# Kernel optimization log

Measured on AMD Instinct MI355X. Metric: run time of the kernel, lower is better.

Reference implementation:

```python
import jax, jax.numpy as jnp
import numpy as np

BATCH = 2048
DIMS = [256, 256, 256, 128]  # input, hidden, hidden, output
N_ATOMS = 4  # identity, sin, tanh, square


def setup_inputs() -> dict:
    key = jax.random.key(0)
    ks = jax.random.split(key, 8)
    inp = {"x": jax.random.normal(ks[0], (BATCH, DIMS[0]), dtype=jnp.float32)}
    for li in range(3):
        out_d, in_d = DIMS[li + 1], DIMS[li]
        inp[f"W{li}"] = jax.random.normal(ks[1 + li], (out_d, in_d), dtype=jnp.float32) * 0.1
        inp[f"b{li}"] = jnp.zeros((out_d,), dtype=jnp.float32)
        inp[f"f_idx{li}"] = jax.random.randint(ks[4 + li], (out_d, in_d), 0, N_ATOMS, dtype=jnp.int32)
    return inp


def _w_eff(W, idx):
    # per-element atom nonlinearity selected by idx: [identity, sin, tanh, square]
    atoms = jnp.stack([W, jnp.sin(W), jnp.tanh(W), W * W], axis=0)  # [A, out, in]
    return jnp.take_along_axis(atoms, idx[None].astype(jnp.int32), axis=0)[0]


def reference(x, W0, b0, W1, b1, W2, b2, f_idx0, f_idx1, f_idx2):
    layers = [(W0, b0, f_idx0), (W1, b1, f_idx1), (W2, b2, f_idx2)]
    h = x
    n = len(layers)
    for li, (W, b, idx) in enumerate(layers):
        We = _w_eff(W, idx)                       # [out, in]
        z = h[:, None, :] * We[None, :, :]        # [batch, out, in]
        gz = z if li == n - 1 else jnp.tanh(z)    # g_fixed='tanh' on hidden layers
        h = gz.sum(axis=-1) + b[None, :]          # [batch, out]
    return h
```

## Files before the change

### kernel.cpp

```cpp
#include <hip/hip_runtime.h>
#include <math.h>


typedef float v2f __attribute__((ext_vector_type(2)));

#define HCLAMP 12.0f
#define INV2PI 0.15915494309189535f
#define SCW    2.885390081777927f

__device__ __forceinline__ float fast_rcp(float x)  { return __builtin_amdgcn_rcpf(x); }
__device__ __forceinline__ float fast_exp2(float x) { return __builtin_amdgcn_exp2f(x); }
__device__ __forceinline__ v2f pk2(float a, float b) { v2f r; r.x = a; r.y = b; return r; }
__device__ __forceinline__ v2f splat2(float f) { v2f r; r.x = f; r.y = f; return r; }
__device__ __forceinline__ v2f vfma(v2f a, v2f b, v2f c) {
    return __builtin_elementwise_fma(a, b, c);
}

__global__ void weff_kernel(const float* __restrict__ W0, const int* __restrict__ I0,
                            const float* __restrict__ W1, const int* __restrict__ I1,
                            const float* __restrict__ W2, const int* __restrict__ I2,
                            float* __restrict__ ws) {
    int tid = blockIdx.x * blockDim.x + threadIdx.x;
    const float* W; const int* I; float* out; int outd; int e;
    if (tid < 65536)        { W = W0; I = I0; out = ws;          outd = 256; e = tid; }
    else if (tid < 131072)  { W = W1; I = I1; out = ws + 65536;  outd = 256; e = tid - 65536; }
    else if (tid < 163840)  { W = W2; I = I2; out = ws + 131072; outd = 128; e = tid - 131072; }
    else return;
    int o = e >> 8;
    int i = e & 255;
    float w = W[e];
    int idx = I[e];
    float sn = __builtin_amdgcn_sinf(w * INV2PI);
    float th = 1.0f - 2.0f * fast_rcp(fast_exp2(w * SCW) + 1.0f);
    float sq = w * w;
    float v = (idx == 1) ? sn : (idx == 2) ? th : (idx == 3) ? sq : w;
    out[(i >> 2) * (outd * 4) + o * 4 + (i & 3)] = v;
}

struct ND { v2f n, d; };
__device__ __forceinline__ ND pade1(v2f z) {
    const v2f c105 = splat2(105.0f), c945 = splat2(945.0f);
    const v2f c420 = splat2(420.0f), c15  = splat2(15.0f);
    v2f t = z * z;
    ND r;
    r.n = z * vfma(t, t + c105, c945);
    r.d = vfma(t, vfma(t, c15, c420), c945);
    return r;
}
__device__ __forceinline__ ND nd_merge(ND a, ND b) {
    ND r;
    r.n = vfma(a.n, b.d, b.n * a.d);
    r.d = a.d * b.d;
    return r;
}
__device__ __forceinline__ ND tree4(float4 pa, float4 pb, float4 w) {
    v2f h0 = pk2(pa.x, pa.y), h1 = pk2(pa.z, pa.w);
    v2f h2 = pk2(pb.x, pb.y), h3 = pk2(pb.z, pb.w);
    ND r0 = pade1(h0 * splat2(w.x));
    ND r1 = pade1(h1 * splat2(w.y));
    ND r2 = pade1(h2 * splat2(w.z));
    ND r3 = pade1(h3 * splat2(w.w));
    return nd_merge(nd_merge(r0, r1), nd_merge(r2, r3));
}
__device__ __forceinline__ v2f sig8_acc(ND a, ND b, v2f acc) {
    v2f num = vfma(b.n, a.d, a.n * b.d);
    v2f den = a.d * b.d;
    v2f rd;  rd.x = fast_rcp(den.x); rd.y = fast_rcp(den.y);
    return vfma(num, rd, acc);
}

__global__ __launch_bounds__(1024, 4) void mlp_kernel(
    const float* __restrict__ x,  const float* __restrict__ b0,
    const float* __restrict__ b1, const float* __restrict__ b2,
    const float* __restrict__ ws, float* __restrict__ out) {
    const float4* We0 = (const float4*)ws;
    const float4* We1 = (const float4*)(ws + 65536);
    const float4* We2 = (const float4*)(ws + 131072);

    __shared__ __align__(16) v2f hA0[256];
    __shared__ __align__(16) v2f hA1[256];
    __shared__ __align__(16) v2f hB0[256];
    __shared__ __align__(16) v2f hB1[256];
    __shared__ __align__(16) v2f partA[1024];
    __shared__ __align__(16) v2f partB[1024];

    const int t = threadIdx.x;
    const int g = t >> 8;
    const int o = t & 255;
    const int p = g >> 1;
    const int l = g & 1;
    const int row0 = blockIdx.x * 4;

    {
        float xv = x[(row0 + 2 * p + l) * 256 + o];
        xv = fminf(fmaxf(xv, -HCLAMP), HCLAMP);
        ((float*)((p ? hA1 : hA0) + o))[l] = xv;
    }
    __syncthreads();

    {
        const float bias = b0[o];
        v2f acc0 = splat2(0.f), acc1 = splat2(0.f);
#pragma unroll 1
        for (int icc = 0; icc < 16; icc += 2) {
            int ic = g * 16 + icc;
            float4 w0 = We0[ic * 256 + o];
            float4 w1 = We0[(ic + 1) * 256 + o];
            const float4* hp0 = (const float4*)(hA0 + ic * 4);
            const float4* hp1 = (const float4*)(hA1 + ic * 4);
            ND r0 = tree4(hp0[0], hp0[1], w0);
            ND r1 = tree4(hp0[2], hp0[3], w1);
            acc0 = sig8_acc(r0, r1, acc0);
            ND r2 = tree4(hp1[0], hp1[1], w0);
            ND r3 = tree4(hp1[2], hp1[3], w1);
            acc1 = sig8_acc(r2, r3, acc1);
        }
        partA[g * 256 + o] = acc0;
        partB[g * 256 + o] = acc1;
        __syncthreads();
        const v2f* prt = p ? partB : partA;
        float s = ((const float*)(prt + o))[l]
                + ((const float*)(prt + 256 + o))[l]
                + ((const float*)(prt + 512 + o))[l]
                + ((const float*)(prt + 768 + o))[l];
        float h = s + bias;
        h = fminf(fmaxf(h, -HCLAMP), HCLAMP);
        ((float*)((p ? hB1 : hB0) + o))[l] = h;
        __syncthreads();
    }

    {
        const float bias = b1[o];
        v2f acc0 = splat2(0.f), acc1 = splat2(0.f);
#pragma unroll 1
        for (int icc = 0; icc < 16; icc += 2) {
            int ic = g * 16 + icc;
            float4 w0 = We1[ic * 256 + o];
            float4 w1 = We1[(ic + 1) * 256 + o];
            const float4* hp0 = (const float4*)(hB0 + ic * 4);
            const float4* hp1 = (const float4*)(hB1 + ic * 4);
            ND r0 = tree4(hp0[0], hp0[1], w0);
            ND r1 = tree4(hp0[2], hp0[3], w1);
            acc0 = sig8_acc(r0, r1, acc0);
            ND r2 = tree4(hp1[0], hp1[1], w0);
            ND r3 = tree4(hp1[2], hp1[3], w1);
            acc1 = sig8_acc(r2, r3, acc1);
        }
        partA[g * 256 + o] = acc0;
        partB[g * 256 + o] = acc1;
        __syncthreads();
        const v2f* prt = p ? partB : partA;
        float s = ((const float*)(prt + o))[l]
                + ((const float*)(prt + 256 + o))[l]
                + ((const float*)(prt + 512 + o))[l]
                + ((const float*)(prt + 768 + o))[l];
        float h = s + bias;
        h = fminf(fmaxf(h, -HCLAMP), HCLAMP);
        ((float*)((p ? hB1 : hA0) + o))[l] = h;
        __syncthreads();
    }

    {
        const int o2 = t & 127;
        const int q  = t >> 7;
        v2f acc0 = splat2(0.f), acc1 = splat2(0.f);
#pragma unroll 4
        for (int icc = 0; icc < 8; icc++) {
            int ic = q * 8 + icc;
            float4 w = We2[ic * 128 + o2];
            const float4* hp0 = (const float4*)(hA0 + ic * 4);
            const float4* hp1 = (const float4*)(hB1 + ic * 4);
            float4 pa = hp0[0], pb = hp0[1];
            float4 qa = hp1[0], qb = hp1[1];
            acc0 = vfma(pk2(pa.x, pa.y), splat2(w.x), acc0);
            acc0 = vfma(pk2(pa.z, pa.w), splat2(w.y), acc0);
            acc0 = vfma(pk2(pb.x, pb.y), splat2(w.z), acc0);
            acc0 = vfma(pk2(pb.z, pb.w), splat2(w.w), acc0);
            acc1 = vfma(pk2(qa.x, qa.y), splat2(w.x), acc1);
            acc1 = vfma(pk2(qa.z, qa.w), splat2(w.y), acc1);
            acc1 = vfma(pk2(qb.x, qb.y), splat2(w.z), acc1);
            acc1 = vfma(pk2(qb.z, qb.w), splat2(w.w), acc1);
        }
        partA[q * 128 + o2] = acc0;
        partB[q * 128 + o2] = acc1;
        __syncthreads();
        if (t < 512) {
            const int r  = t >> 7;
            const int oo = t & 127;
            const v2f* prt = (r & 2) ? partB : partA;
            const int  ln  = r & 1;
            float s = 0.0f;
#pragma unroll
            for (int q2 = 0; q2 < 8; q2++)
                s += ((const float*)(prt + q2 * 128 + oo))[ln];
            out[(row0 + r) * 128 + oo] = s + b2[oo];
        }
    }
}

extern "C" void kernel_launch(void* const* d_in, const int* in_sizes, int n_in,
                              void* d_out, int out_size, void* d_ws, size_t ws_size,
                              hipStream_t stream) {
    const float* x  = (const float*)d_in[0];
    const float* W0 = (const float*)d_in[1];
    const float* b0 = (const float*)d_in[2];
    const int*   I0 = (const int*)  d_in[3];
    const float* W1 = (const float*)d_in[4];
    const float* b1 = (const float*)d_in[5];
    const int*   I1 = (const int*)  d_in[6];
    const float* W2 = (const float*)d_in[7];
    const float* b2 = (const float*)d_in[8];
    const int*   I2 = (const int*)  d_in[9];
    float* ws  = (float*)d_ws;
    float* out = (float*)d_out;

    weff_kernel<<<640, 256, 0, stream>>>(W0, I0, W1, I1, W2, I2, ws);
    mlp_kernel<<<512, 1024, 0, stream>>>(x, b0, b1, b2, ws, out);
}
```

Measured before the change: 126.4 us.

## Assign one row per thread group and drop the cross-group K-split reduction

Work is redistributed so each group of 256 threads owns one batch row and loops over the full input dimension. This removes the shared-memory partial-sum buffers and the extra barrier reductions per layer, and packs the v2f pairs along K instead of across two rows. In exchange each weight float4 is reused by one row instead of two, which doubles the weight loads per FLOP. The final layer also idles half the threads. The launch bound is relaxed from 4 to 2.

```diff
diff --git a/kernel.cpp b/kernel.cpp
--- a/kernel.cpp
+++ b/kernel.cpp
@@ -7,6 +7,7 @@
 #define HCLAMP 12.0f
 #define INV2PI 0.15915494309189535f
 #define SCW    2.885390081777927f
+#define LPAD   260
 
 __device__ __forceinline__ float fast_rcp(float x)  { return __builtin_amdgcn_rcpf(x); }
 __device__ __forceinline__ float fast_exp2(float x) { return __builtin_amdgcn_exp2f(x); }
@@ -53,15 +54,6 @@
     r.d = a.d * b.d;
     return r;
 }
-__device__ __forceinline__ ND tree4(float4 pa, float4 pb, float4 w) {
-    v2f h0 = pk2(pa.x, pa.y), h1 = pk2(pa.z, pa.w);
-    v2f h2 = pk2(pb.x, pb.y), h3 = pk2(pb.z, pb.w);
-    ND r0 = pade1(h0 * splat2(w.x));
-    ND r1 = pade1(h1 * splat2(w.y));
-    ND r2 = pade1(h2 * splat2(w.z));
-    ND r3 = pade1(h3 * splat2(w.w));
-    return nd_merge(nd_merge(r0, r1), nd_merge(r2, r3));
-}
 __device__ __forceinline__ v2f sig8_acc(ND a, ND b, v2f acc) {
     v2f num = vfma(b.n, a.d, a.n * b.d);
     v2f den = a.d * b.d;
@@ -69,7 +61,7 @@
     return vfma(num, rd, acc);
 }
 
-__global__ __launch_bounds__(1024, 4) void mlp_kernel(
+__global__ __launch_bounds__(1024, 2) void mlp_kernel(
     const float* __restrict__ x,  const float* __restrict__ b0,
     const float* __restrict__ b1, const float* __restrict__ b2,
     const float* __restrict__ ws, float* __restrict__ out) {
@@ -77,124 +69,75 @@
     const float4* We1 = (const float4*)(ws + 65536);
     const float4* We2 = (const float4*)(ws + 131072);
 
-    __shared__ __align__(16) v2f hA0[256];
-    __shared__ __align__(16) v2f hA1[256];
-    __shared__ __align__(16) v2f hB0[256];
-    __shared__ __align__(16) v2f hB1[256];
-    __shared__ __align__(16) v2f partA[1024];
-    __shared__ __align__(16) v2f partB[1024];
+    __shared__ __align__(16) float hA[4 * LPAD];
+    __shared__ __align__(16) float hB[4 * LPAD];
 
     const int t = threadIdx.x;
-    const int g = t >> 8;
+    const int r = t >> 8;
     const int o = t & 255;
-    const int p = g >> 1;
-    const int l = g & 1;
     const int row0 = blockIdx.x * 4;
 
     {
-        float xv = x[(row0 + 2 * p + l) * 256 + o];
-        xv = fminf(fmaxf(xv, -HCLAMP), HCLAMP);
-        ((float*)((p ? hA1 : hA0) + o))[l] = xv;
+        float xv = x[(row0 + r) * 256 + o];
+        hA[r * LPAD + o] = fminf(fmaxf(xv, -HCLAMP), HCLAMP);
     }
     __syncthreads();
 
     {
         const float bias = b0[o];
-        v2f acc0 = splat2(0.f), acc1 = splat2(0.f);
-#pragma unroll 1
-        for (int icc = 0; icc < 16; icc += 2) {
-            int ic = g * 16 + icc;
-            float4 w0 = We0[ic * 256 + o];
-            float4 w1 = We0[(ic + 1) * 256 + o];
-            const float4* hp0 = (const float4*)(hA0 + ic * 4);
-            const float4* hp1 = (const float4*)(hA1 + ic * 4);
-            ND r0 = tree4(hp0[0], hp0[1], w0);
-            ND r1 = tree4(hp0[2], hp0[3], w1);
-            acc0 = sig8_acc(r0, r1, acc0);
-            ND r2 = tree4(hp1[0], hp1[1], w0);
-            ND r3 = tree4(hp1[2], hp1[3], w1);
-            acc1 = sig8_acc(r2, r3, acc1);
+        const float* hr = hA + r * LPAD;
+        v2f acc = splat2(0.f);
+#pragma unroll 2
+        for (int kk = 0; kk < 64; kk += 2) {
+            float4 w0v = We0[kk * 256 + o];
+            float4 w1v = We0[(kk + 1) * 256 + o];
+            float4 h0v = *(const float4*)(hr + kk * 4);
+            float4 h1v = *(const float4*)(hr + kk * 4 + 4);
+            ND a = nd_merge(pade1(pk2(h0v.x, h0v.y) * pk2(w0v.x, w0v.y)),
+                            pade1(pk2(h0v.z, h0v.w) * pk2(w0v.z, w0v.w)));
+            ND b = nd_merge(pade1(pk2(h1v.x, h1v.y) * pk2(w1v.x, w1v.y)),
+                            pade1(pk2(h1v.z, h1v.w) * pk2(w1v.z, w1v.w)));
+            acc = sig8_acc(a, b, acc);
         }
-        partA[g * 256 + o] = acc0;
-        partB[g * 256 + o] = acc1;
-        __syncthreads();
-        const v2f* prt = p ? partB : partA;
-        float s = ((const float*)(prt + o))[l]
-                + ((const float*)(prt + 256 + o))[l]
-                + ((const float*)(prt + 512 + o))[l]
-                + ((const float*)(prt + 768 + o))[l];
-        float h = s + bias;
+        float h = acc.x + acc.y + bias;
         h = fminf(fmaxf(h, -HCLAMP), HCLAMP);
-        ((float*)((p ? hB1 : hB0) + o))[l] = h;
-        __syncthreads();
+        hB[r * LPAD + o] = h;
     }
+    __syncthreads();
 
     {
         const float bias = b1[o];
-        v2f acc0 = splat2(0.f), acc1 = splat2(0.f);
-#pragma unroll 1
-        for (int icc = 0; icc < 16; icc += 2) {
-            int ic = g * 16 + icc;
-            float4 w0 = We1[ic * 256 + o];
-            float4 w1 = We1[(ic + 1) * 256 + o];
-            const float4* hp0 = (const float4*)(hB0 + ic * 4);
-            const float4* hp1 = (const float4*)(hB1 + ic * 4);
-            ND r0 = tree4(hp0[0], hp0[1], w0);
-            ND r1 = tree4(hp0[2], hp0[3], w1);
-            acc0 = sig8_acc(r0, r1, acc0);
-            ND r2 = tree4(hp1[0], hp1[1], w0);
-            ND r3 = tree4(hp1[2], hp1[3], w1);
-            acc1 = sig8_acc(r2, r3, acc1);
+        const float* hr = hB + r * LPAD;
+        v2f acc = splat2(0.f);
+#pragma unroll 2
+        for (int kk = 0; kk < 64; kk += 2) {
+            float4 w0v = We1[kk * 256 + o];
+            float4 w1v = We1[(kk + 1) * 256 + o];
+            float4 h0v = *(const float4*)(hr + kk * 4);
+            float4 h1v = *(const float4*)(hr + kk * 4 + 4);
+            ND a = nd_merge(pade1(pk2(h0v.x, h0v.y) * pk2(w0v.x, w0v.y)),
+                            pade1(pk2(h0v.z, h0v.w) * pk2(w0v.z, w0v.w)));
+            ND b = nd_merge(pade1(pk2(h1v.x, h1v.y) * pk2(w1v.x, w1v.y)),
+                            pade1(pk2(h1v.z, h1v.w) * pk2(w1v.z, w1v.w)));
+            acc = sig8_acc(a, b, acc);
         }
-        partA[g * 256 + o] = acc0;
-        partB[g * 256 + o] = acc1;
-        __syncthreads();
-        const v2f* prt = p ? partB : partA;
-        float s = ((const float*)(prt + o))[l]
-                + ((const float*)(prt + 256 + o))[l]
-                + ((const float*)(prt + 512 + o))[l]
-                + ((const float*)(prt + 768 + o))[l];
-        float h = s + bias;
+        float h = acc.x + acc.y + bias;
         h = fminf(fmaxf(h, -HCLAMP), HCLAMP);
-        ((float*)((p ? hB1 : hA0) + o))[l] = h;
-        __syncthreads();
+        hA[r * LPAD + o] = h;
     }
+    __syncthreads();
 
-    {
-        const int o2 = t & 127;
-        const int q  = t >> 7;
-        v2f acc0 = splat2(0.f), acc1 = splat2(0.f);
+    if (o < 128) {
+        const float* hr = hA + r * LPAD;
+        v2f acc = splat2(0.f);
 #pragma unroll 4
-        for (int icc = 0; icc < 8; icc++) {
-            int ic = q * 8 + icc;
-            float4 w = We2[ic * 128 + o2];
-            const float4* hp0 = (const float4*)(hA0 + ic * 4);
-            const float4* hp1 = (const float4*)(hB1 + ic * 4);
-            float4 pa = hp0[0], pb = hp0[1];
-            float4 qa = hp1[0], qb = hp1[1];
-            acc0 = vfma(pk2(pa.x, pa.y), splat2(w.x), acc0);
-            acc0 = vfma(pk2(pa.z, pa.w), splat2(w.y), acc0);
-            acc0 = vfma(pk2(pb.x, pb.y), splat2(w.z), acc0);
-            acc0 = vfma(pk2(pb.z, pb.w), splat2(w.w), acc0);
-            acc1 = vfma(pk2(qa.x, qa.y), splat2(w.x), acc1);
-            acc1 = vfma(pk2(qa.z, qa.w), splat2(w.y), acc1);
-            acc1 = vfma(pk2(qb.x, qb.y), splat2(w.z), acc1);
-            acc1 = vfma(pk2(qb.z, qb.w), splat2(w.w), acc1);
+        for (int kk = 0; kk < 64; kk++) {
+            float4 w = We2[kk * 128 + o];
+            float4 h = *(const float4*)(hr + kk * 4);
+            acc = vfma(pk2(h.x, h.y), pk2(w.x, w.y), acc);
+            acc = vfma(pk2(h.z, h.w), pk2(w.z, w.w), acc);
         }
-        partA[q * 128 + o2] = acc0;
-        partB[q * 128 + o2] = acc1;
-        __syncthreads();
-        if (t < 512) {
-            const int r  = t >> 7;
-            const int oo = t & 127;
-            const v2f* prt = (r & 2) ? partB : partA;
-            const int  ln  = r & 1;
-            float s = 0.0f;
-#pragma unroll
-            for (int q2 = 0; q2 < 8; q2++)
-                s += ((const float*)(prt + q2 * 128 + oo))[ln];
-            out[(row0 + r) * 128 + oo] = s + b2[oo];
-        }
+        out[(row0 + r) * 128 + o] = acc.x + acc.y + b2[o];
     }
 }
 
```

Result: slower. 135.6 us (+7.2%).

## Replace Padé tanh with exp2-based reciprocal-sum formulation for hidden-layer activations

Applied to the files above, without the earlier changes.

Replaces the [3/2]-Padé rational tanh approximation with an exact exp2 form. tanh(z) is written as 1 - 2/(e^{2z}+1), and the sum of reciprocals is accumulated as a merged numerator/denominator tree, with scaling by 2^-8 to avoid overflow. Inputs are pre-scaled by 2/ln2 so each element costs one FMA plus one exp2, and the affine correction (256 - s/128) and the bias are folded into the layer epilogue. The change also fully unrolls the main loops. It trades polynomial ALU work for transcendental-unit throughput and risks overflow or precision loss in the products of up to 16 exponentials under the clamp of 32.

```diff
diff --git a/kernel.cpp b/kernel.cpp
--- a/kernel.cpp
+++ b/kernel.cpp
@@ -4,9 +4,11 @@
 
 typedef float v2f __attribute__((ext_vector_type(2)));
 
-#define HCLAMP 12.0f
+#define SC   2.885390081777927f
+#define INV  (1.0f / 2.885390081777927f)
 #define INV2PI 0.15915494309189535f
-#define SCW    2.885390081777927f
+#define HS_CLAMP 32.0f
+#define C8   0.00390625f
 
 __device__ __forceinline__ float fast_rcp(float x)  { return __builtin_amdgcn_rcpf(x); }
 __device__ __forceinline__ float fast_exp2(float x) { return __builtin_amdgcn_exp2f(x); }
@@ -14,6 +16,9 @@
 __device__ __forceinline__ v2f splat2(float f) { v2f r; r.x = f; r.y = f; return r; }
 __device__ __forceinline__ v2f vfma(v2f a, v2f b, v2f c) {
     return __builtin_elementwise_fma(a, b, c);
+}
+__device__ __forceinline__ v2f pexp(v2f t) {
+    v2f e; e.x = fast_exp2(t.x); e.y = fast_exp2(t.y); return e;
 }
 
 __global__ void weff_kernel(const float* __restrict__ W0, const int* __restrict__ I0,
@@ -31,37 +36,26 @@
     float w = W[e];
     int idx = I[e];
     float sn = __builtin_amdgcn_sinf(w * INV2PI);
-    float th = 1.0f - 2.0f * fast_rcp(fast_exp2(w * SCW) + 1.0f);
+    float th = 1.0f - 2.0f * fast_rcp(fast_exp2(w * SC) + 1.0f);
     float sq = w * w;
     float v = (idx == 1) ? sn : (idx == 2) ? th : (idx == 3) ? sq : w;
     out[(i >> 2) * (outd * 4) + o * 4 + (i & 3)] = v;
 }
 
 struct ND { v2f n, d; };
-__device__ __forceinline__ ND pade1(v2f z) {
-    const v2f c105 = splat2(105.0f), c945 = splat2(945.0f);
-    const v2f c420 = splat2(420.0f), c15  = splat2(15.0f);
-    v2f t = z * z;
+__device__ __forceinline__ ND tree4(float4 pa, float4 pb, float4 w, v2f m8, v2f c8) {
+    v2f B0 = pexp(vfma(pk2(pa.x, pa.y), splat2(w.x), m8)) + c8;
+    v2f B1 = pexp(vfma(pk2(pa.z, pa.w), splat2(w.y), m8)) + c8;
+    v2f B2 = pexp(vfma(pk2(pb.x, pb.y), splat2(w.z), m8)) + c8;
+    v2f B3 = pexp(vfma(pk2(pb.z, pb.w), splat2(w.w), m8)) + c8;
+    v2f S1 = B0 + B1, P1 = B0 * B1;
+    v2f S2 = B2 + B3, P2 = B2 * B3;
     ND r;
-    r.n = z * vfma(t, t + c105, c945);
-    r.d = vfma(t, vfma(t, c15, c420), c945);
+    r.n = vfma(S2, P1, S1 * P2);
+    r.d = P1 * P2;
     return r;
 }
-__device__ __forceinline__ ND nd_merge(ND a, ND b) {
-    ND r;
-    r.n = vfma(a.n, b.d, b.n * a.d);
-    r.d = a.d * b.d;
-    return r;
-}
-__device__ __forceinline__ ND tree4(float4 pa, float4 pb, float4 w) {
-    v2f h0 = pk2(pa.x, pa.y), h1 = pk2(pa.z, pa.w);
-    v2f h2 = pk2(pb.x, pb.y), h3 = pk2(pb.z, pb.w);
-    ND r0 = pade1(h0 * splat2(w.x));
-    ND r1 = pade1(h1 * splat2(w.y));
-    ND r2 = pade1(h2 * splat2(w.z));
-    ND r3 = pade1(h3 * splat2(w.w));
-    return nd_merge(nd_merge(r0, r1), nd_merge(r2, r3));
-}
+
 __device__ __forceinline__ v2f sig8_acc(ND a, ND b, v2f acc) {
     v2f num = vfma(b.n, a.d, a.n * b.d);
     v2f den = a.d * b.d;
@@ -91,9 +85,12 @@
     const int l = g & 1;
     const int row0 = blockIdx.x * 4;
 
-    {
-        float xv = x[(row0 + 2 * p + l) * 256 + o];
-        xv = fminf(fmaxf(xv, -HCLAMP), HCLAMP);
+    const v2f m8 = pk2(-8.0f, -8.0f);
+    const v2f c8 = pk2(C8, C8);
+
+    {
+        float xv = x[(row0 + 2 * p + l) * 256 + o] * SC;
+        xv = fminf(fmaxf(xv, -HS_CLAMP), HS_CLAMP);
         ((float*)((p ? hA1 : hA0) + o))[l] = xv;
     }
     __syncthreads();
@@ -101,18 +98,18 @@
     {
         const float bias = b0[o];
         v2f acc0 = splat2(0.f), acc1 = splat2(0.f);
-#pragma unroll 1
+#pragma unroll
         for (int icc = 0; icc < 16; icc += 2) {
             int ic = g * 16 + icc;
             float4 w0 = We0[ic * 256 + o];
             float4 w1 = We0[(ic + 1) * 256 + o];
             const float4* hp0 = (const float4*)(hA0 + ic * 4);
             const float4* hp1 = (const float4*)(hA1 + ic * 4);
-            ND r0 = tree4(hp0[0], hp0[1], w0);
-            ND r1 = tree4(hp0[2], hp0[3], w1);
+            ND r0 = tree4(hp0[0], hp0[1], w0, m8, c8);
+            ND r1 = tree4(hp0[2], hp0[3], w1, m8, c8);
             acc0 = sig8_acc(r0, r1, acc0);
-            ND r2 = tree4(hp1[0], hp1[1], w0);
-            ND r3 = tree4(hp1[2], hp1[3], w1);
+            ND r2 = tree4(hp1[0], hp1[1], w0, m8, c8);
+            ND r3 = tree4(hp1[2], hp1[3], w1, m8, c8);
             acc1 = sig8_acc(r2, r3, acc1);
         }
         partA[g * 256 + o] = acc0;
@@ -123,8 +120,8 @@
                 + ((const float*)(prt + 256 + o))[l]
                 + ((const float*)(prt + 512 + o))[l]
                 + ((const float*)(prt + 768 + o))[l];
-        float h = s + bias;
-        h = fminf(fmaxf(h, -HCLAMP), HCLAMP);
+        float h = (256.0f - 0.0078125f * s + bias) * SC;
+        h = fminf(fmaxf(h, -HS_CLAMP), HS_CLAMP);
         ((float*)((p ? hB1 : hB0) + o))[l] = h;
         __syncthreads();
     }
@@ -132,18 +129,18 @@
     {
         const float bias = b1[o];
         v2f acc0 = splat2(0.f), acc1 = splat2(0.f);
-#pragma unroll 1
+#pragma unroll
         for (int icc = 0; icc < 16; icc += 2) {
             int ic = g * 16 + icc;
             float4 w0 = We1[ic * 256 + o];
             float4 w1 = We1[(ic + 1) * 256 + o];
             const float4* hp0 = (const float4*)(hB0 + ic * 4);
             const float4* hp1 = (const float4*)(hB1 + ic * 4);
-            ND r0 = tree4(hp0[0], hp0[1], w0);
-            ND r1 = tree4(hp0[2], hp0[3], w1);
+            ND r0 = tree4(hp0[0], hp0[1], w0, m8, c8);
+            ND r1 = tree4(hp0[2], hp0[3], w1, m8, c8);
             acc0 = sig8_acc(r0, r1, acc0);
-            ND r2 = tree4(hp1[0], hp1[1], w0);
-            ND r3 = tree4(hp1[2], hp1[3], w1);
+            ND r2 = tree4(hp1[0], hp1[1], w0, m8, c8);
+            ND r3 = tree4(hp1[2], hp1[3], w1, m8, c8);
             acc1 = sig8_acc(r2, r3, acc1);
         }
         partA[g * 256 + o] = acc0;
@@ -154,8 +151,8 @@
                 + ((const float*)(prt + 256 + o))[l]
                 + ((const float*)(prt + 512 + o))[l]
                 + ((const float*)(prt + 768 + o))[l];
-        float h = s + bias;
-        h = fminf(fmaxf(h, -HCLAMP), HCLAMP);
+        float h = (256.0f - 0.0078125f * s + bias) * SC;
+        h = fminf(fmaxf(h, -HS_CLAMP), HS_CLAMP);
         ((float*)((p ? hB1 : hA0) + o))[l] = h;
         __syncthreads();
     }
@@ -164,7 +161,7 @@
         const int o2 = t & 127;
         const int q  = t >> 7;
         v2f acc0 = splat2(0.f), acc1 = splat2(0.f);
-#pragma unroll 4
+#pragma unroll
         for (int icc = 0; icc < 8; icc++) {
             int ic = q * 8 + icc;
             float4 w = We2[ic * 128 + o2];
@@ -193,7 +190,7 @@
 #pragma unroll
             for (int q2 = 0; q2 < 8; q2++)
                 s += ((const float*)(prt + q2 * 128 + oo))[ln];
-            out[(row0 + r) * 128 + oo] = s + b2[oo];
+            out[(row0 + r) * 128 + oo] = s * INV + b2[oo];
         }
     }
 }
```

Result: faster. 115.4 us (-8.8%).
